# Kernel tuning notes

Measured on AMD Instinct MI355X. Metric: run time of the kernel, lower is better.

## Reference

```python
import jax, jax.numpy as jnp
import numpy as np

ROWS = 256
COLS = 256
EPS = 1e-8


def _radius_bins(rows, cols):
    # Same construction as SpectralLoss.__init__: integer radius per rfft bin,
    # ifftshifted along the row axis to match torch.rfft layout.
    shift_rows = rows // 2
    cols_onesided = cols // 2 + 1
    idx = np.indices((rows, cols_onesided)) - np.array([[[shift_rows]], [[0]]])
    r = np.sqrt(idx[0] ** 2 + idx[1] ** 2).astype(int)
    r = np.fft.ifftshift(r, axes=0)
    return r  # [rows, cols_onesided], values in [0, r_max]


def setup_inputs() -> dict:
    key = jax.random.key(0)
    k1, k2 = jax.random.split(key)
    r = _radius_bins(ROWS, COLS)
    vector_length = int(r.max()) + 1  # 182
    data = jax.random.normal(k1, (128, 3, ROWS, COLS), dtype=jnp.float32)
    mean = jax.random.uniform(k2, (vector_length,), dtype=jnp.float32)
    radius = jnp.asarray(r, dtype=jnp.int32)
    return {"data": data, "mean": mean, "radius": radius}


def reference(data, mean, radius):
    L = mean.shape[0]  # vector_length = r_max + 1
    # RGB -> luma (as in SpectralLoss.fft)
    gray = 0.299 * data[:, 0] + 0.587 * data[:, 1] + 0.114 * data[:, 2]  # [B,H,W]
    f = jnp.fft.rfft2(gray)  # [B, H, W//2+1]
    power = f.real ** 2 + f.imag ** 2  # sum of squared re/im parts
    fft_abs = 20.0 * jnp.log(power + EPS)  # [B, H, Wc]
    # Radial histogram: segment-mean keyed on integer radius (replaces the
    # original dense one-hot mask broadcast of shape [B, L, H, Wc]).
    seg = radius.reshape(-1)  # [N] with N = H*Wc
    B = fft_abs.shape[0]
    flat = fft_abs.reshape(B, -1).T  # [N, B]
    sums = jax.ops.segment_sum(flat, seg, num_segments=L)  # [L, B]
    counts = jax.ops.segment_sum(jnp.ones_like(flat[:, :1]), seg, num_segments=L)  # [L, 1]
    profile = (sums / counts).T  # [B, L]
    # Per-sample min-max normalization (same order of ops as torch code)
    profile = profile - jnp.min(profile, axis=1, keepdims=True)
    profile = profile / jnp.max(profile, axis=1, keepdims=True)
    # L1 loss with reduction='sum' against the target mean profile
    return jnp.sum(jnp.abs(profile - mean[None, :]))
```

## Files before the change

### kernel.cpp

```cpp
#include <hip/hip_runtime.h>
#include <cmath>

#define B_   128
#define H_   256
#define W_   256
#define WC_  129
#define L_   182
#define NG_  33
#define PI_F 3.14159265358979f

__device__ __forceinline__ void fft256_wave(float vr[4], float vi[4], int l) {
  float c0, s0;
  __sincosf(-2.f * PI_F * (float)l / 256.f, &s0, &c0);
  {
    float ur = vr[0] + vr[2], ui = vi[0] + vi[2];
    float dr = vr[0] - vr[2], di = vi[0] - vi[2];
    vr[0] = ur; vi[0] = ui;
    vr[2] = dr * c0 - di * s0; vi[2] = dr * s0 + di * c0;
    float c1 = s0, s1 = -c0;
    ur = vr[1] + vr[3]; ui = vi[1] + vi[3];
    dr = vr[1] - vr[3]; di = vi[1] - vi[3];
    vr[1] = ur; vi[1] = ui;
    vr[3] = dr * c1 - di * s1; vi[3] = dr * s1 + di * c1;
  }
  {
    float c2 = c0 * c0 - s0 * s0, s2 = 2.f * c0 * s0;
    float ur = vr[0] + vr[1], ui = vi[0] + vi[1];
    float dr = vr[0] - vr[1], di = vi[0] - vi[1];
    vr[0] = ur; vi[0] = ui;
    vr[1] = dr * c2 - di * s2; vi[1] = dr * s2 + di * c2;
    ur = vr[2] + vr[3]; ui = vi[2] + vi[3];
    dr = vr[2] - vr[3]; di = vi[2] - vi[3];
    vr[2] = ur; vi[2] = ui;
    vr[3] = dr * c2 - di * s2; vi[3] = dr * s2 + di * c2;
  }
  #pragma unroll
  for (int h = 32; h >= 1; h >>= 1) {
    int i = l & (h - 1);
    float c, s;
    __sincosf(-PI_F * (float)i / (float)h, &s, &c);
    bool up = (l & h) != 0;
    float cc = up ? c : 1.f;
    float ss = up ? s : 0.f;
    float sgn = up ? -1.f : 1.f;
    #pragma unroll
    for (int j = 0; j < 4; ++j) {
      float br = __shfl_xor(vr[j], h, 64);
      float bi = __shfl_xor(vi[j], h, 64);
      float tr = fmaf(sgn, vr[j], br);
      float ti = fmaf(sgn, vi[j], bi);
      vr[j] = tr * cc - ti * ss;
      vi[j] = tr * ss + ti * cc;
    }
  }
}

__device__ __forceinline__ void stage4(float (&vr)[4][4], float (&vi)[4][4],
                                       int l, int h, float CT, float ST) {
  int i = l & (h - 1);
  float s, c;
  __sincosf(-PI_F * (float)i / (float)h, &s, &c);
  float wr[4], wi[4];
  wr[0] = c;                    wi[0] = s;
  wr[1] = c * CT + s * ST;      wi[1] = s * CT - c * ST;
  wr[2] = wr[1] * CT + wi[1] * ST; wi[2] = wi[1] * CT - wr[1] * ST;
  wr[3] = wr[2] * CT + wi[2] * ST; wi[3] = wi[2] * CT - wr[2] * ST;
  bool up = (l & h) != 0;
  float sgn = up ? -1.f : 1.f;
  #pragma unroll
  for (int f = 0; f < 4; ++f) {
    #pragma unroll
    for (int j = 0; j < 4; ++j) {
      float br = __shfl_xor(vr[f][j], h, 64);
      float bi = __shfl_xor(vi[f][j], h, 64);
      float tr = fmaf(sgn, vr[f][j], br);
      float ti = fmaf(sgn, vi[f][j], bi);
      float cc = up ? wr[j] : 1.f;
      float ss = up ? wi[j] : 0.f;
      vr[f][j] = tr * cc - ti * ss;
      vi[f][j] = tr * ss + ti * cc;
    }
  }
}

__device__ __forceinline__ float4 luma4(float4 r, float4 g, float4 b) {
  float4 o;
  o.x = fmaf(0.299f, r.x, fmaf(0.587f, g.x, 0.114f * b.x));
  o.y = fmaf(0.299f, r.y, fmaf(0.587f, g.y, 0.114f * b.y));
  o.z = fmaf(0.299f, r.z, fmaf(0.587f, g.z, 0.114f * b.z));
  o.w = fmaf(0.299f, r.w, fmaf(0.587f, g.w, 0.114f * b.w));
  return o;
}

#define P1_STRIDE 259

__global__ __launch_bounds__(256) void pass1_kernel(
    const float* __restrict__ data, float4* __restrict__ inter4) {
  __shared__ float2 tile[16 * P1_STRIDE];
  int tid = threadIdx.x;
  int w = tid >> 6, l = tid & 63;
  int b = blockIdx.x >> 3;
  int rg = blockIdx.x & 7;
  int row0 = rg * 32;
  const float* img = data + ((size_t)b * 3) * (H_ * W_);
  float vr[4][4], vi[4][4];
  #pragma unroll
  for (int half = 0; half < 2; ++half) {
    float4 ra[2], ga[2], ba[2], rb[2], gb[2], bb[2];
    #pragma unroll
    for (int e = 0; e < 2; ++e) {
      int f = half * 2 + e;
      int rowA = row0 + 2 * (4 * w + f);
      const float* pA = img + (size_t)rowA * W_ + 4 * l;
      ra[e] = *(const float4*)(pA);
      ga[e] = *(const float4*)(pA + H_ * W_);
      ba[e] = *(const float4*)(pA + 2 * H_ * W_);
      rb[e] = *(const float4*)(pA + W_);
      gb[e] = *(const float4*)(pA + H_ * W_ + W_);
      bb[e] = *(const float4*)(pA + 2 * H_ * W_ + W_);
    }
    #pragma unroll
    for (int e = 0; e < 2; ++e) {
      int f = half * 2 + e;
      float4 A = luma4(ra[e], ga[e], ba[e]);
      float4 Bv = luma4(rb[e], gb[e], bb[e]);
      vr[f][0] = A.x; vr[f][1] = A.y; vr[f][2] = A.z; vr[f][3] = A.w;
      vi[f][0] = Bv.x; vi[f][1] = Bv.y; vi[f][2] = Bv.z; vi[f][3] = Bv.w;
    }
  }
  stage4(vr, vi, l, 32, 0.9996988187f, 0.0245412285f);
  stage4(vr, vi, l, 16, 0.9987954562f, 0.0490676743f);
  stage4(vr, vi, l,  8, 0.9951847267f, 0.0980171403f);
  stage4(vr, vi, l,  4, 0.9807852804f, 0.1950903220f);
  stage4(vr, vi, l,  2, 0.9238795325f, 0.3826834324f);
  stage4(vr, vi, l,  1, 0.7071067812f, 0.7071067812f);
  #pragma unroll
  for (int f = 0; f < 4; ++f) {
    float u0r = vr[f][0] + vr[f][2], u0i = vi[f][0] + vi[f][2];
    float v0r = vr[f][0] - vr[f][2], v0i = vi[f][0] - vi[f][2];
    float u1r = vr[f][1] + vr[f][3], u1i = vi[f][1] + vi[f][3];
    float d1r = vr[f][1] - vr[f][3], d1i = vi[f][1] - vi[f][3];
    float v1r = d1i, v1i = -d1r;
    vr[f][0] = u0r + u1r; vi[f][0] = u0i + u1i;
    vr[f][1] = u0r - u1r; vi[f][1] = u0i - u1i;
    vr[f][2] = v0r + v1r; vi[f][2] = v0i + v1i;
    vr[f][3] = v0r - v1r; vi[f][3] = v0i - v1i;
    int p = 4 * w + f;
    #pragma unroll
    for (int j = 0; j < 4; ++j)
      tile[p * P1_STRIDE + l + 64 * j] = make_float2(vr[f][j], vi[f][j]);
  }
  __syncthreads();
  for (int fi = tid; fi < WC_ * 16; fi += 256) {
    int k = fi >> 4;
    int p = fi & 15;
    int q  = (int)(__brev((unsigned)k) >> 24);
    int qn = (int)(__brev((unsigned)((256 - k) & 255)) >> 24);
    int qs  = (q >> 2)  + 64 * (q & 3);
    int qns = (qn >> 2) + 64 * (qn & 3);
    float2 Zk  = tile[p * P1_STRIDE + qs];
    float2 Znk = tile[p * P1_STRIDE + qns];
    float4 o;
    o.x = 0.5f * (Zk.x + Znk.x);
    o.y = 0.5f * (Zk.y - Znk.y);
    o.z = 0.5f * (Zk.y + Znk.y);
    o.w = 0.5f * (Znk.x - Zk.x);
    inter4[((((size_t)b * WC_ + k) * H_ + row0) >> 1) + p] = o;
  }
}

__global__ __launch_bounds__(256) void pass2_kernel(
    const float2* __restrict__ inter, const int* __restrict__ radius,
    float* __restrict__ partial, float* __restrict__ cntpart) {
  __shared__ float lbins[L_];
  __shared__ float lcnt[L_];
  int tid = threadIdx.x;
  int wv = tid >> 6, l = tid & 63;
  int b = blockIdx.x / NG_;
  int g = blockIdx.x - b * NG_;
  int k = g * 4 + wv;
  bool do_cnt = (b == 0);
  for (int i = tid; i < L_; i += 256) lbins[i] = 0.f;
  if (do_cnt)
    for (int i = tid; i < L_; i += 256) lcnt[i] = 0.f;
  __syncthreads();
  if (k < WC_) {
    const float2* p = inter + ((size_t)b * WC_ + k) * H_;
    float vr[4], vi[4];
    #pragma unroll
    for (int j = 0; j < 4; ++j) {
      float2 v = p[l + 64 * j];
      vr[j] = v.x; vi[j] = v.y;
    }
    fft256_wave(vr, vi, l);
    int rb = 4 * (int)(__brev((unsigned)l) >> 26);
    #pragma unroll
    for (int j = 0; j < 4; ++j) {
      int rf = rb + ((j == 1) ? 2 : (j == 2) ? 1 : j);
      int bin = radius[rf * WC_ + k];
      float pw = vr[j] * vr[j] + vi[j] * vi[j];
      float val = 20.f * __logf(pw + 1e-8f);
      atomicAdd(&lbins[bin], val);
      if (do_cnt) atomicAdd(&lcnt[bin], 1.f);
    }
  }
  __syncthreads();
  float* pp = partial + ((size_t)b * NG_ + g) * L_;
  for (int i = tid; i < L_; i += 256) pp[i] = lbins[i];
  if (do_cnt) {
    float* cp = cntpart + (size_t)g * L_;
    for (int i = tid; i < L_; i += 256) cp[i] = lcnt[i];
  }
}

__global__ __launch_bounds__(256) void loss_kernel(
    const float* __restrict__ partial, const float* __restrict__ cntpart,
    const float* __restrict__ mean, float* __restrict__ lpart) {
  int b = blockIdx.x;
  int t = threadIdx.x;
  __shared__ float prof[L_];
  __shared__ float red[256];
  float acc = 0.f, csum = 0.f;
  if (t < L_) {
    const float* pb = partial + (size_t)b * NG_ * L_;
    #pragma unroll 3
    for (int g = 0; g < NG_; ++g) {
      acc  += pb[g * L_ + t];
      csum += cntpart[g * L_ + t];
    }
    prof[t] = acc / csum;
  }
  __syncthreads();
  red[t] = (t < L_) ? prof[t] : INFINITY;
  __syncthreads();
  for (int s = 128; s > 0; s >>= 1) {
    if (t < s) red[t] = fminf(red[t], red[t + s]);
    __syncthreads();
  }
  float mn = red[0];
  __syncthreads();
  red[t] = (t < L_) ? (prof[t] - mn) : -INFINITY;
  __syncthreads();
  for (int s = 128; s > 0; s >>= 1) {
    if (t < s) red[t] = fmaxf(red[t], red[t + s]);
    __syncthreads();
  }
  float mx = red[0];
  __syncthreads();
  red[t] = (t < L_) ? fabsf((prof[t] - mn) / mx - mean[t]) : 0.f;
  __syncthreads();
  for (int s = 128; s > 0; s >>= 1) {
    if (t < s) red[t] += red[t + s];
    __syncthreads();
  }
  if (t == 0) lpart[b] = red[0];
}

__global__ __launch_bounds__(64) void final_kernel(
    const float* __restrict__ lpart, float* __restrict__ out) {
  int l = threadIdx.x;
  float v = lpart[l] + lpart[l + 64];
  #pragma unroll
  for (int h = 32; h >= 1; h >>= 1) v += __shfl_xor(v, h, 64);
  if (l == 0) out[0] = v;
}

extern "C" void kernel_launch(void* const* d_in, const int* in_sizes, int n_in,
                              void* d_out, int out_size, void* d_ws, size_t ws_size,
                              hipStream_t stream) {
  const float* data   = (const float*)d_in[0];
  const float* mean   = (const float*)d_in[1];
  const int*   radius = (const int*)d_in[2];
  float* out = (float*)d_out;

  float2* inter = (float2*)d_ws;
  size_t inter_bytes = (size_t)B_ * WC_ * H_ * sizeof(float2);
  float* partial = (float*)((char*)d_ws + inter_bytes);
  float* cntpart = partial + (size_t)B_ * NG_ * L_;
  float* lpart   = cntpart + (size_t)NG_ * L_;

  pass1_kernel<<<B_ * 8, 256, 0, stream>>>(data, (float4*)inter);
  pass2_kernel<<<B_ * NG_, 256, 0, stream>>>(inter, radius, partial, cntpart);
  loss_kernel<<<B_, 256, 0, stream>>>(partial, cntpart, mean, lpart);
  final_kernel<<<1, 64, 0, stream>>>(lpart, out);
}
```

Before: 196.8 us.

## Fuse row and column FFT passes into one kernel using shared-memory transpose

New measurement: 219.9 us. 1.12x slower.

```diff
diff --git a/kernel.cpp b/kernel.cpp
--- a/kernel.cpp
+++ b/kernel.cpp
@@ -6,54 +6,10 @@
 #define W_   256
 #define WC_  129
 #define L_   182
-#define NG_  33
 #define PI_F 3.14159265358979f
 
-__device__ __forceinline__ void fft256_wave(float vr[4], float vi[4], int l) {
-  float c0, s0;
-  __sincosf(-2.f * PI_F * (float)l / 256.f, &s0, &c0);
-  {
-    float ur = vr[0] + vr[2], ui = vi[0] + vi[2];
-    float dr = vr[0] - vr[2], di = vi[0] - vi[2];
-    vr[0] = ur; vi[0] = ui;
-    vr[2] = dr * c0 - di * s0; vi[2] = dr * s0 + di * c0;
-    float c1 = s0, s1 = -c0;
-    ur = vr[1] + vr[3]; ui = vi[1] + vi[3];
-    dr = vr[1] - vr[3]; di = vi[1] - vi[3];
-    vr[1] = ur; vi[1] = ui;
-    vr[3] = dr * c1 - di * s1; vi[3] = dr * s1 + di * c1;
-  }
-  {
-    float c2 = c0 * c0 - s0 * s0, s2 = 2.f * c0 * s0;
-    float ur = vr[0] + vr[1], ui = vi[0] + vi[1];
-    float dr = vr[0] - vr[1], di = vi[0] - vi[1];
-    vr[0] = ur; vi[0] = ui;
-    vr[1] = dr * c2 - di * s2; vi[1] = dr * s2 + di * c2;
-    ur = vr[2] + vr[3]; ui = vi[2] + vi[3];
-    dr = vr[2] - vr[3]; di = vi[2] - vi[3];
-    vr[2] = ur; vi[2] = ui;
-    vr[3] = dr * c2 - di * s2; vi[3] = dr * s2 + di * c2;
-  }
-  #pragma unroll
-  for (int h = 32; h >= 1; h >>= 1) {
-    int i = l & (h - 1);
-    float c, s;
-    __sincosf(-PI_F * (float)i / (float)h, &s, &c);
-    bool up = (l & h) != 0;
-    float cc = up ? c : 1.f;
-    float ss = up ? s : 0.f;
-    float sgn = up ? -1.f : 1.f;
-    #pragma unroll
-    for (int j = 0; j < 4; ++j) {
-      float br = __shfl_xor(vr[j], h, 64);
-      float bi = __shfl_xor(vi[j], h, 64);
-      float tr = fmaf(sgn, vr[j], br);
-      float ti = fmaf(sgn, vi[j], bi);
-      vr[j] = tr * cc - ti * ss;
-      vi[j] = tr * ss + ti * cc;
-    }
-  }
-}
+#define COLS_ELEMS (128 * 65)
+#define SMEM_BYTES (COLS_ELEMS * 16 + 2 * L_ * 4)
 
 __device__ __forceinline__ void stage4(float (&vr)[4][4], float (&vi)[4][4],
                                        int l, int h, float CT, float ST) {
@@ -61,8 +17,8 @@
   float s, c;
   __sincosf(-PI_F * (float)i / (float)h, &s, &c);
   float wr[4], wi[4];
-  wr[0] = c;                    wi[0] = s;
-  wr[1] = c * CT + s * ST;      wi[1] = s * CT - c * ST;
+  wr[0] = c;                       wi[0] = s;
+  wr[1] = c * CT + s * ST;         wi[1] = s * CT - c * ST;
   wr[2] = wr[1] * CT + wi[1] * ST; wi[2] = wi[1] * CT - wr[1] * ST;
   wr[3] = wr[2] * CT + wi[2] * ST; wi[3] = wi[2] * CT - wr[2] * ST;
   bool up = (l & h) != 0;
@@ -83,51 +39,8 @@
   }
 }
 
-__device__ __forceinline__ float4 luma4(float4 r, float4 g, float4 b) {
-  float4 o;
-  o.x = fmaf(0.299f, r.x, fmaf(0.587f, g.x, 0.114f * b.x));
-  o.y = fmaf(0.299f, r.y, fmaf(0.587f, g.y, 0.114f * b.y));
-  o.z = fmaf(0.299f, r.z, fmaf(0.587f, g.z, 0.114f * b.z));
-  o.w = fmaf(0.299f, r.w, fmaf(0.587f, g.w, 0.114f * b.w));
-  return o;
-}
-
-#define P1_STRIDE 259
-
-__global__ __launch_bounds__(256) void pass1_kernel(
-    const float* __restrict__ data, float4* __restrict__ inter4) {
-  __shared__ float2 tile[16 * P1_STRIDE];
-  int tid = threadIdx.x;
-  int w = tid >> 6, l = tid & 63;
-  int b = blockIdx.x >> 3;
-  int rg = blockIdx.x & 7;
-  int row0 = rg * 32;
-  const float* img = data + ((size_t)b * 3) * (H_ * W_);
-  float vr[4][4], vi[4][4];
-  #pragma unroll
-  for (int half = 0; half < 2; ++half) {
-    float4 ra[2], ga[2], ba[2], rb[2], gb[2], bb[2];
-    #pragma unroll
-    for (int e = 0; e < 2; ++e) {
-      int f = half * 2 + e;
-      int rowA = row0 + 2 * (4 * w + f);
-      const float* pA = img + (size_t)rowA * W_ + 4 * l;
-      ra[e] = *(const float4*)(pA);
-      ga[e] = *(const float4*)(pA + H_ * W_);
-      ba[e] = *(const float4*)(pA + 2 * H_ * W_);
-      rb[e] = *(const float4*)(pA + W_);
-      gb[e] = *(const float4*)(pA + H_ * W_ + W_);
-      bb[e] = *(const float4*)(pA + 2 * H_ * W_ + W_);
-    }
-    #pragma unroll
-    for (int e = 0; e < 2; ++e) {
-      int f = half * 2 + e;
-      float4 A = luma4(ra[e], ga[e], ba[e]);
-      float4 Bv = luma4(rb[e], gb[e], bb[e]);
-      vr[f][0] = A.x; vr[f][1] = A.y; vr[f][2] = A.z; vr[f][3] = A.w;
-      vi[f][0] = Bv.x; vi[f][1] = Bv.y; vi[f][2] = Bv.z; vi[f][3] = Bv.w;
-    }
-  }
+__device__ __forceinline__ void fft256x4(float (&vr)[4][4], float (&vi)[4][4],
+                                         int l) {
   stage4(vr, vi, l, 32, 0.9996988187f, 0.0245412285f);
   stage4(vr, vi, l, 16, 0.9987954562f, 0.0490676743f);
   stage4(vr, vi, l,  8, 0.9951847267f, 0.0980171403f);
@@ -145,71 +58,135 @@
     vr[f][1] = u0r - u1r; vi[f][1] = u0i - u1i;
     vr[f][2] = v0r + v1r; vi[f][2] = v0i + v1i;
     vr[f][3] = v0r - v1r; vi[f][3] = v0i - v1i;
-    int p = 4 * w + f;
-    #pragma unroll
-    for (int j = 0; j < 4; ++j)
-      tile[p * P1_STRIDE + l + 64 * j] = make_float2(vr[f][j], vi[f][j]);
-  }
-  __syncthreads();
-  for (int fi = tid; fi < WC_ * 16; fi += 256) {
-    int k = fi >> 4;
-    int p = fi & 15;
-    int q  = (int)(__brev((unsigned)k) >> 24);
-    int qn = (int)(__brev((unsigned)((256 - k) & 255)) >> 24);
-    int qs  = (q >> 2)  + 64 * (q & 3);
-    int qns = (qn >> 2) + 64 * (qn & 3);
-    float2 Zk  = tile[p * P1_STRIDE + qs];
-    float2 Znk = tile[p * P1_STRIDE + qns];
-    float4 o;
-    o.x = 0.5f * (Zk.x + Znk.x);
-    o.y = 0.5f * (Zk.y - Znk.y);
-    o.z = 0.5f * (Zk.y + Znk.y);
-    o.w = 0.5f * (Znk.x - Zk.x);
-    inter4[((((size_t)b * WC_ + k) * H_ + row0) >> 1) + p] = o;
-  }
-}
-
-__global__ __launch_bounds__(256) void pass2_kernel(
-    const float2* __restrict__ inter, const int* __restrict__ radius,
+  }
+}
+
+__device__ __forceinline__ float4 luma4(float4 r, float4 g, float4 b) {
+  float4 o;
+  o.x = fmaf(0.299f, r.x, fmaf(0.587f, g.x, 0.114f * b.x));
+  o.y = fmaf(0.299f, r.y, fmaf(0.587f, g.y, 0.114f * b.y));
+  o.z = fmaf(0.299f, r.z, fmaf(0.587f, g.z, 0.114f * b.z));
+  o.w = fmaf(0.299f, r.w, fmaf(0.587f, g.w, 0.114f * b.w));
+  return o;
+}
+
+__global__ __launch_bounds__(1024) void fused_kernel(
+    const float* __restrict__ data, const int* __restrict__ radius,
     float* __restrict__ partial, float* __restrict__ cntpart) {
-  __shared__ float lbins[L_];
-  __shared__ float lcnt[L_];
+  extern __shared__ char smem[];
+  float4* cols4 = (float4*)smem;
+  float* lbins = (float*)(smem + COLS_ELEMS * 16);
+  float* lcnt  = lbins + L_;
+
   int tid = threadIdx.x;
-  int wv = tid >> 6, l = tid & 63;
-  int b = blockIdx.x / NG_;
-  int g = blockIdx.x - b * NG_;
-  int k = g * 4 + wv;
-  bool do_cnt = (b == 0);
-  for (int i = tid; i < L_; i += 256) lbins[i] = 0.f;
-  if (do_cnt)
-    for (int i = tid; i < L_; i += 256) lcnt[i] = 0.f;
-  __syncthreads();
-  if (k < WC_) {
-    const float2* p = inter + ((size_t)b * WC_ + k) * H_;
-    float vr[4], vi[4];
-    #pragma unroll
-    for (int j = 0; j < 4; ++j) {
-      float2 v = p[l + 64 * j];
-      vr[j] = v.x; vi[j] = v.y;
-    }
-    fft256_wave(vr, vi, l);
-    int rb = 4 * (int)(__brev((unsigned)l) >> 26);
-    #pragma unroll
-    for (int j = 0; j < 4; ++j) {
-      int rf = rb + ((j == 1) ? 2 : (j == 2) ? 1 : j);
-      int bin = radius[rf * WC_ + k];
-      float pw = vr[j] * vr[j] + vi[j] * vi[j];
-      float val = 20.f * __logf(pw + 1e-8f);
-      atomicAdd(&lbins[bin], val);
-      if (do_cnt) atomicAdd(&lcnt[bin], 1.f);
-    }
-  }
-  __syncthreads();
-  float* pp = partial + ((size_t)b * NG_ + g) * L_;
-  for (int i = tid; i < L_; i += 256) pp[i] = lbins[i];
+  int w = tid >> 6, l = tid & 63;
+  int bid = blockIdx.x;
+  int b = bid >> 1;
+  int half = bid & 1;
+  int k0h = half ? 65 : 0;
+  int klcount = half ? 64 : 65;
+  bool do_cnt = (bid < 2);
+
+  for (int i = tid; i < L_; i += 1024) { lbins[i] = 0.f; lcnt[i] = 0.f; }
+
+  const float* img = data + ((size_t)b * 3) * (H_ * W_);
+  const int m = (int)(__brev((unsigned)l) >> 26);
+  const int m2 = (64 - m) & 63;
+  const int l2 = (int)(__brev((unsigned)m2) >> 26);
+  const int amap[4] = {0, 2, 1, 3};
+
+  #pragma unroll
+  for (int bt = 0; bt < 2; ++bt) {
+    float vr[4][4], vi[4][4];
+    #pragma unroll
+    for (int hb = 0; hb < 2; ++hb) {
+      float4 ra[2], ga[2], ba[2], rb[2], gb[2], bb[2];
+      #pragma unroll
+      for (int e = 0; e < 2; ++e) {
+        int f = hb * 2 + e;
+        int p = w * 8 + bt * 4 + f;
+        const float* pA = img + (size_t)(2 * p) * W_ + 4 * l;
+        ra[e] = *(const float4*)(pA);
+        ga[e] = *(const float4*)(pA + H_ * W_);
+        ba[e] = *(const float4*)(pA + 2 * H_ * W_);
+        rb[e] = *(const float4*)(pA + W_);
+        gb[e] = *(const float4*)(pA + H_ * W_ + W_);
+        bb[e] = *(const float4*)(pA + 2 * H_ * W_ + W_);
+      }
+      #pragma unroll
+      for (int e = 0; e < 2; ++e) {
+        int f = hb * 2 + e;
+        float4 A = luma4(ra[e], ga[e], ba[e]);
+        float4 Bv = luma4(rb[e], gb[e], bb[e]);
+        vr[f][0] = A.x; vr[f][1] = A.y; vr[f][2] = A.z; vr[f][3] = A.w;
+        vi[f][0] = Bv.x; vi[f][1] = Bv.y; vi[f][2] = Bv.z; vi[f][3] = Bv.w;
+      }
+    }
+    fft256x4(vr, vi, l);
+    #pragma unroll
+    for (int f = 0; f < 4; ++f) {
+      int p = w * 8 + bt * 4 + f;
+      #pragma unroll
+      for (int j = 0; j < 3; ++j) {
+        int k = (amap[j] << 6) | m;
+        float pr = __shfl(vr[f][3 - j], l2, 64);
+        float pi = __shfl(vi[f][3 - j], l2, 64);
+        if (l == 0) {
+          int js = (j < 2) ? j : (5 - j);
+          pr = vr[f][js]; pi = vi[f][js];
+        }
+        int kl = k - k0h;
+        if (kl >= 0 && kl < klcount) {
+          float4 o;
+          o.x = 0.5f * (vr[f][j] + pr);
+          o.y = 0.5f * (vi[f][j] - pi);
+          o.z = 0.5f * (vi[f][j] + pi);
+          o.w = 0.5f * (pr - vr[f][j]);
+          cols4[p * 65 + kl] = o;
+        }
+      }
+    }
+  }
+  __syncthreads();
+
+  int tmax = (klcount + 3) >> 2;
+  for (int t = w; t < tmax; t += 16) {
+    float vr[4][4], vi[4][4];
+    #pragma unroll
+    for (int ff = 0; ff < 4; ++ff) {
+      int kl = 4 * t + ff;
+      int klr = (kl < klcount) ? kl : 0;
+      float4 c0 = cols4[(2 * l) * 65 + klr];
+      float4 c1 = cols4[(2 * l + 1) * 65 + klr];
+      vr[ff][0] = c0.x; vi[ff][0] = c0.y;
+      vr[ff][1] = c0.z; vi[ff][1] = c0.w;
+      vr[ff][2] = c1.x; vi[ff][2] = c1.y;
+      vr[ff][3] = c1.z; vi[ff][3] = c1.w;
+    }
+    fft256x4(vr, vi, l);
+    #pragma unroll
+    for (int ff = 0; ff < 4; ++ff) {
+      int kl = 4 * t + ff;
+      if (kl < klcount) {
+        int kabs = k0h + kl;
+        #pragma unroll
+        for (int j = 0; j < 4; ++j) {
+          int frow = (amap[j] << 6) | m;
+          int bin = radius[frow * WC_ + kabs];
+          float pw = vr[ff][j] * vr[ff][j] + vi[ff][j] * vi[ff][j];
+          float val = 20.f * __logf(pw + 1e-8f);
+          atomicAdd(&lbins[bin], val);
+          if (do_cnt) atomicAdd(&lcnt[bin], 1.f);
+        }
+      }
+    }
+  }
+  __syncthreads();
+  float* pp = partial + (size_t)bid * L_;
+  for (int i = tid; i < L_; i += 1024) pp[i] = lbins[i];
   if (do_cnt) {
-    float* cp = cntpart + (size_t)g * L_;
-    for (int i = tid; i < L_; i += 256) cp[i] = lcnt[i];
+    float* cp = cntpart + (size_t)half * L_;
+    for (int i = tid; i < L_; i += 1024) cp[i] = lcnt[i];
   }
 }
 
@@ -220,14 +197,10 @@
   int t = threadIdx.x;
   __shared__ float prof[L_];
   __shared__ float red[256];
-  float acc = 0.f, csum = 0.f;
   if (t < L_) {
-    const float* pb = partial + (size_t)b * NG_ * L_;
-    #pragma unroll 3
-    for (int g = 0; g < NG_; ++g) {
-      acc  += pb[g * L_ + t];
-      csum += cntpart[g * L_ + t];
-    }
+    float acc  = partial[(size_t)(b * 2) * L_ + t] +
+                 partial[(size_t)(b * 2 + 1) * L_ + t];
+    float csum = cntpart[t] + cntpart[L_ + t];
     prof[t] = acc / csum;
   }
   __syncthreads();
@@ -273,14 +246,15 @@
   const int*   radius = (const int*)d_in[2];
   float* out = (float*)d_out;
 
-  float2* inter = (float2*)d_ws;
-  size_t inter_bytes = (size_t)B_ * WC_ * H_ * sizeof(float2);
-  float* partial = (float*)((char*)d_ws + inter_bytes);
-  float* cntpart = partial + (size_t)B_ * NG_ * L_;
-  float* lpart   = cntpart + (size_t)NG_ * L_;
-
-  pass1_kernel<<<B_ * 8, 256, 0, stream>>>(data, (float4*)inter);
-  pass2_kernel<<<B_ * NG_, 256, 0, stream>>>(inter, radius, partial, cntpart);
+  float* partial = (float*)d_ws;
+  float* cntpart = partial + (size_t)256 * L_;
+  float* lpart   = cntpart + 2 * L_;
+
+  (void)hipFuncSetAttribute((const void*)fused_kernel,
+                            hipFuncAttributeMaxDynamicSharedMemorySize,
+                            SMEM_BYTES);
+
+  fused_kernel<<<B_ * 2, 1024, SMEM_BYTES, stream>>>(data, radius, partial, cntpart);
   loss_kernel<<<B_, 256, 0, stream>>>(partial, cntpart, mean, lpart);
   final_kernel<<<1, 64, 0, stream>>>(lpart, out);
 }
```

## Store FFT intermediate in fp16, batch column FFTs, fuse loss into pass2

Applied to the files above, without the earlier changes.

Result: slower. 299.9 us (+52.4%).

```diff
diff --git a/kernel.cpp b/kernel.cpp
--- a/kernel.cpp
+++ b/kernel.cpp
@@ -6,54 +6,11 @@
 #define W_   256
 #define WC_  129
 #define L_   182
-#define NG_  33
+#define NG_  9
 #define PI_F 3.14159265358979f
 
-__device__ __forceinline__ void fft256_wave(float vr[4], float vi[4], int l) {
-  float c0, s0;
-  __sincosf(-2.f * PI_F * (float)l / 256.f, &s0, &c0);
-  {
-    float ur = vr[0] + vr[2], ui = vi[0] + vi[2];
-    float dr = vr[0] - vr[2], di = vi[0] - vi[2];
-    vr[0] = ur; vi[0] = ui;
-    vr[2] = dr * c0 - di * s0; vi[2] = dr * s0 + di * c0;
-    float c1 = s0, s1 = -c0;
-    ur = vr[1] + vr[3]; ui = vi[1] + vi[3];
-    dr = vr[1] - vr[3]; di = vi[1] - vi[3];
-    vr[1] = ur; vi[1] = ui;
-    vr[3] = dr * c1 - di * s1; vi[3] = dr * s1 + di * c1;
-  }
-  {
-    float c2 = c0 * c0 - s0 * s0, s2 = 2.f * c0 * s0;
-    float ur = vr[0] + vr[1], ui = vi[0] + vi[1];
-    float dr = vr[0] - vr[1], di = vi[0] - vi[1];
-    vr[0] = ur; vi[0] = ui;
-    vr[1] = dr * c2 - di * s2; vi[1] = dr * s2 + di * c2;
-    ur = vr[2] + vr[3]; ui = vi[2] + vi[3];
-    dr = vr[2] - vr[3]; di = vi[2] - vi[3];
-    vr[2] = ur; vi[2] = ui;
-    vr[3] = dr * c2 - di * s2; vi[3] = dr * s2 + di * c2;
-  }
-  #pragma unroll
-  for (int h = 32; h >= 1; h >>= 1) {
-    int i = l & (h - 1);
-    float c, s;
-    __sincosf(-PI_F * (float)i / (float)h, &s, &c);
-    bool up = (l & h) != 0;
-    float cc = up ? c : 1.f;
-    float ss = up ? s : 0.f;
-    float sgn = up ? -1.f : 1.f;
-    #pragma unroll
-    for (int j = 0; j < 4; ++j) {
-      float br = __shfl_xor(vr[j], h, 64);
-      float bi = __shfl_xor(vi[j], h, 64);
-      float tr = fmaf(sgn, vr[j], br);
-      float ti = fmaf(sgn, vi[j], bi);
-      vr[j] = tr * cc - ti * ss;
-      vi[j] = tr * ss + ti * cc;
-    }
-  }
-}
+using half4 = __attribute__((ext_vector_type(4))) _Float16;
+using half8 = __attribute__((ext_vector_type(8))) _Float16;
 
 __device__ __forceinline__ void stage4(float (&vr)[4][4], float (&vi)[4][4],
                                        int l, int h, float CT, float ST) {
@@ -61,8 +18,8 @@
   float s, c;
   __sincosf(-PI_F * (float)i / (float)h, &s, &c);
   float wr[4], wi[4];
-  wr[0] = c;                    wi[0] = s;
-  wr[1] = c * CT + s * ST;      wi[1] = s * CT - c * ST;
+  wr[0] = c;                       wi[0] = s;
+  wr[1] = c * CT + s * ST;         wi[1] = s * CT - c * ST;
   wr[2] = wr[1] * CT + wi[1] * ST; wi[2] = wi[1] * CT - wr[1] * ST;
   wr[3] = wr[2] * CT + wi[2] * ST; wi[3] = wi[2] * CT - wr[2] * ST;
   bool up = (l & h) != 0;
@@ -83,6 +40,28 @@
   }
 }
 
+__device__ __forceinline__ void fft256x4(float (&vr)[4][4], float (&vi)[4][4],
+                                         int l) {
+  stage4(vr, vi, l, 32, 0.9996988187f, 0.0245412285f);
+  stage4(vr, vi, l, 16, 0.9987954562f, 0.0490676743f);
+  stage4(vr, vi, l,  8, 0.9951847267f, 0.0980171403f);
+  stage4(vr, vi, l,  4, 0.9807852804f, 0.1950903220f);
+  stage4(vr, vi, l,  2, 0.9238795325f, 0.3826834324f);
+  stage4(vr, vi, l,  1, 0.7071067812f, 0.7071067812f);
+  #pragma unroll
+  for (int f = 0; f < 4; ++f) {
+    float u0r = vr[f][0] + vr[f][2], u0i = vi[f][0] + vi[f][2];
+    float v0r = vr[f][0] - vr[f][2], v0i = vi[f][0] - vi[f][2];
+    float u1r = vr[f][1] + vr[f][3], u1i = vi[f][1] + vi[f][3];
+    float d1r = vr[f][1] - vr[f][3], d1i = vi[f][1] - vi[f][3];
+    float v1r = d1i, v1i = -d1r;
+    vr[f][0] = u0r + u1r; vi[f][0] = u0i + u1i;
+    vr[f][1] = u0r - u1r; vi[f][1] = u0i - u1i;
+    vr[f][2] = v0r + v1r; vi[f][2] = v0i + v1i;
+    vr[f][3] = v0r - v1r; vi[f][3] = v0i - v1i;
+  }
+}
+
 __device__ __forceinline__ float4 luma4(float4 r, float4 g, float4 b) {
   float4 o;
   o.x = fmaf(0.299f, r.x, fmaf(0.587f, g.x, 0.114f * b.x));
@@ -95,9 +74,14 @@
 #define P1_STRIDE 259
 
 __global__ __launch_bounds__(256) void pass1_kernel(
-    const float* __restrict__ data, float4* __restrict__ inter4) {
+    const float* __restrict__ data, half4* __restrict__ interh,
+    const int* __restrict__ radius, float* __restrict__ cnt,
+    int* __restrict__ counters) {
   __shared__ float2 tile[16 * P1_STRIDE];
+  __shared__ float lcnt[L_];
   int tid = threadIdx.x;
+  bool blk0 = (blockIdx.x == 0);
+  if (blk0 && tid < L_) lcnt[tid] = 0.f;
   int w = tid >> 6, l = tid & 63;
   int b = blockIdx.x >> 3;
   int rg = blockIdx.x & 7;
@@ -128,23 +112,9 @@
       vi[f][0] = Bv.x; vi[f][1] = Bv.y; vi[f][2] = Bv.z; vi[f][3] = Bv.w;
     }
   }
-  stage4(vr, vi, l, 32, 0.9996988187f, 0.0245412285f);
-  stage4(vr, vi, l, 16, 0.9987954562f, 0.0490676743f);
-  stage4(vr, vi, l,  8, 0.9951847267f, 0.0980171403f);
-  stage4(vr, vi, l,  4, 0.9807852804f, 0.1950903220f);
-  stage4(vr, vi, l,  2, 0.9238795325f, 0.3826834324f);
-  stage4(vr, vi, l,  1, 0.7071067812f, 0.7071067812f);
+  fft256x4(vr, vi, l);
   #pragma unroll
   for (int f = 0; f < 4; ++f) {
-    float u0r = vr[f][0] + vr[f][2], u0i = vi[f][0] + vi[f][2];
-    float v0r = vr[f][0] - vr[f][2], v0i = vi[f][0] - vi[f][2];
-    float u1r = vr[f][1] + vr[f][3], u1i = vi[f][1] + vi[f][3];
-    float d1r = vr[f][1] - vr[f][3], d1i = vi[f][1] - vi[f][3];
-    float v1r = d1i, v1i = -d1r;
-    vr[f][0] = u0r + u1r; vi[f][0] = u0i + u1i;
-    vr[f][1] = u0r - u1r; vi[f][1] = u0i - u1i;
-    vr[f][2] = v0r + v1r; vi[f][2] = v0i + v1i;
-    vr[f][3] = v0r - v1r; vi[f][3] = v0i - v1i;
     int p = 4 * w + f;
     #pragma unroll
     for (int j = 0; j < 4; ++j)
@@ -160,109 +130,126 @@
     int qns = (qn >> 2) + 64 * (qn & 3);
     float2 Zk  = tile[p * P1_STRIDE + qs];
     float2 Znk = tile[p * P1_STRIDE + qns];
-    float4 o;
-    o.x = 0.5f * (Zk.x + Znk.x);
-    o.y = 0.5f * (Zk.y - Znk.y);
-    o.z = 0.5f * (Zk.y + Znk.y);
-    o.w = 0.5f * (Znk.x - Zk.x);
-    inter4[((((size_t)b * WC_ + k) * H_ + row0) >> 1) + p] = o;
+    half4 o;
+    o[0] = (_Float16)(0.5f * (Zk.x + Znk.x));
+    o[1] = (_Float16)(0.5f * (Zk.y - Znk.y));
+    o[2] = (_Float16)(0.5f * (Zk.y + Znk.y));
+    o[3] = (_Float16)(0.5f * (Znk.x - Zk.x));
+    interh[((size_t)b * WC_ + k) * 128 + rg * 16 + p] = o;
+  }
+  if (blk0) {
+    __syncthreads();
+    int base = tid * 129;
+    int end  = base + 129;
+    if (end > H_ * WC_) end = H_ * WC_;
+    for (int i = base; i < end; ++i) atomicAdd(&lcnt[radius[i]], 1.f);
+    __syncthreads();
+    if (tid < L_) cnt[tid] = lcnt[tid];
+    if (tid < B_ + 1) counters[tid] = 0;
   }
 }
 
 __global__ __launch_bounds__(256) void pass2_kernel(
-    const float2* __restrict__ inter, const int* __restrict__ radius,
-    float* __restrict__ partial, float* __restrict__ cntpart) {
+    const half8* __restrict__ interh8, const int* __restrict__ radius,
+    const float* __restrict__ cnt, const float* __restrict__ mean,
+    float* __restrict__ partial, float* __restrict__ lpart,
+    int* __restrict__ counters, float* __restrict__ out) {
   __shared__ float lbins[L_];
-  __shared__ float lcnt[L_];
+  __shared__ float prof[L_];
+  __shared__ float red[256];
+  __shared__ int flag;
   int tid = threadIdx.x;
   int wv = tid >> 6, l = tid & 63;
   int b = blockIdx.x / NG_;
   int g = blockIdx.x - b * NG_;
-  int k = g * 4 + wv;
-  bool do_cnt = (b == 0);
   for (int i = tid; i < L_; i += 256) lbins[i] = 0.f;
-  if (do_cnt)
-    for (int i = tid; i < L_; i += 256) lcnt[i] = 0.f;
-  __syncthreads();
-  if (k < WC_) {
-    const float2* p = inter + ((size_t)b * WC_ + k) * H_;
-    float vr[4], vi[4];
-    #pragma unroll
-    for (int j = 0; j < 4; ++j) {
-      float2 v = p[l + 64 * j];
-      vr[j] = v.x; vi[j] = v.y;
-    }
-    fft256_wave(vr, vi, l);
-    int rb = 4 * (int)(__brev((unsigned)l) >> 26);
-    #pragma unroll
-    for (int j = 0; j < 4; ++j) {
-      int rf = rb + ((j == 1) ? 2 : (j == 2) ? 1 : j);
-      int bin = radius[rf * WC_ + k];
-      float pw = vr[j] * vr[j] + vi[j] * vi[j];
-      float val = 20.f * __logf(pw + 1e-8f);
-      atomicAdd(&lbins[bin], val);
-      if (do_cnt) atomicAdd(&lcnt[bin], 1.f);
+  __syncthreads();
+
+  const int amap[4] = {0, 2, 1, 3};
+  const int m = (int)(__brev((unsigned)l) >> 26);
+  float vr[4][4], vi[4][4];
+  int kc[4];
+  #pragma unroll
+  for (int ff = 0; ff < 4; ++ff) {
+    int k = g * 16 + wv * 4 + ff;
+    kc[ff] = k;
+    int kr = (k < WC_) ? k : 0;
+    half8 hx = interh8[((size_t)b * WC_ + kr) * 64 + l];
+    vr[ff][0] = (float)hx[0]; vi[ff][0] = (float)hx[1];
+    vr[ff][1] = (float)hx[2]; vi[ff][1] = (float)hx[3];
+    vr[ff][2] = (float)hx[4]; vi[ff][2] = (float)hx[5];
+    vr[ff][3] = (float)hx[6]; vi[ff][3] = (float)hx[7];
+  }
+  fft256x4(vr, vi, l);
+  #pragma unroll
+  for (int ff = 0; ff < 4; ++ff) {
+    if (kc[ff] < WC_) {
+      #pragma unroll
+      for (int j = 0; j < 4; ++j) {
+        int frow = (amap[j] << 6) | m;
+        int bin = radius[frow * WC_ + kc[ff]];
+        float pw = vr[ff][j] * vr[ff][j] + vi[ff][j] * vi[ff][j];
+        atomicAdd(&lbins[bin], 20.f * __logf(pw + 1e-8f));
+      }
     }
   }
   __syncthreads();
   float* pp = partial + ((size_t)b * NG_ + g) * L_;
   for (int i = tid; i < L_; i += 256) pp[i] = lbins[i];
-  if (do_cnt) {
-    float* cp = cntpart + (size_t)g * L_;
-    for (int i = tid; i < L_; i += 256) cp[i] = lcnt[i];
-  }
-}
-
-__global__ __launch_bounds__(256) void loss_kernel(
-    const float* __restrict__ partial, const float* __restrict__ cntpart,
-    const float* __restrict__ mean, float* __restrict__ lpart) {
-  int b = blockIdx.x;
-  int t = threadIdx.x;
-  __shared__ float prof[L_];
-  __shared__ float red[256];
-  float acc = 0.f, csum = 0.f;
-  if (t < L_) {
+
+  if (tid == 0) {
+    __threadfence();
+    flag = (atomicAdd(&counters[b], 1) == NG_ - 1) ? 1 : 0;
+  }
+  __syncthreads();
+  if (!flag) return;
+  __threadfence();
+  if (tid < L_) {
     const float* pb = partial + (size_t)b * NG_ * L_;
-    #pragma unroll 3
-    for (int g = 0; g < NG_; ++g) {
-      acc  += pb[g * L_ + t];
-      csum += cntpart[g * L_ + t];
-    }
-    prof[t] = acc / csum;
-  }
-  __syncthreads();
-  red[t] = (t < L_) ? prof[t] : INFINITY;
-  __syncthreads();
-  for (int s = 128; s > 0; s >>= 1) {
-    if (t < s) red[t] = fminf(red[t], red[t + s]);
+    float acc = 0.f;
+    #pragma unroll
+    for (int gg = 0; gg < NG_; ++gg) acc += pb[gg * L_ + tid];
+    prof[tid] = acc / cnt[tid];
+  }
+  __syncthreads();
+  red[tid] = (tid < L_) ? prof[tid] : INFINITY;
+  __syncthreads();
+  for (int s = 128; s > 0; s >>= 1) {
+    if (tid < s) red[tid] = fminf(red[tid], red[tid + s]);
     __syncthreads();
   }
   float mn = red[0];
   __syncthreads();
-  red[t] = (t < L_) ? (prof[t] - mn) : -INFINITY;
-  __syncthreads();
-  for (int s = 128; s > 0; s >>= 1) {
-    if (t < s) red[t] = fmaxf(red[t], red[t + s]);
+  red[tid] = (tid < L_) ? (prof[tid] - mn) : -INFINITY;
+  __syncthreads();
+  for (int s = 128; s > 0; s >>= 1) {
+    if (tid < s) red[tid] = fmaxf(red[tid], red[tid + s]);
     __syncthreads();
   }
   float mx = red[0];
   __syncthreads();
-  red[t] = (t < L_) ? fabsf((prof[t] - mn) / mx - mean[t]) : 0.f;
-  __syncthreads();
-  for (int s = 128; s > 0; s >>= 1) {
-    if (t < s) red[t] += red[t + s];
-    __syncthreads();
-  }
-  if (t == 0) lpart[b] = red[0];
-}
-
-__global__ __launch_bounds__(64) void final_kernel(
-    const float* __restrict__ lpart, float* __restrict__ out) {
-  int l = threadIdx.x;
-  float v = lpart[l] + lpart[l + 64];
-  #pragma unroll
-  for (int h = 32; h >= 1; h >>= 1) v += __shfl_xor(v, h, 64);
-  if (l == 0) out[0] = v;
+  red[tid] = (tid < L_) ? fabsf((prof[tid] - mn) / mx - mean[tid]) : 0.f;
+  __syncthreads();
+  for (int s = 128; s > 0; s >>= 1) {
+    if (tid < s) red[tid] += red[tid + s];
+    __syncthreads();
+  }
+  if (tid == 0) lpart[b] = red[0];
+
+  if (tid == 0) {
+    __threadfence();
+    flag = (atomicAdd(&counters[B_], 1) == B_ - 1) ? 1 : 0;
+  }
+  __syncthreads();
+  if (!flag) return;
+  __threadfence();
+  red[tid] = (tid < B_) ? lpart[tid] : 0.f;
+  __syncthreads();
+  for (int s = 128; s > 0; s >>= 1) {
+    if (tid < s) red[tid] += red[tid + s];
+    __syncthreads();
+  }
+  if (tid == 0) out[0] = red[0];
 }
 
 extern "C" void kernel_launch(void* const* d_in, const int* in_sizes, int n_in,
@@ -273,14 +260,14 @@
   const int*   radius = (const int*)d_in[2];
   float* out = (float*)d_out;
 
-  float2* inter = (float2*)d_ws;
-  size_t inter_bytes = (size_t)B_ * WC_ * H_ * sizeof(float2);
-  float* partial = (float*)((char*)d_ws + inter_bytes);
-  float* cntpart = partial + (size_t)B_ * NG_ * L_;
-  float* lpart   = cntpart + (size_t)NG_ * L_;
-
-  pass1_kernel<<<B_ * 8, 256, 0, stream>>>(data, (float4*)inter);
-  pass2_kernel<<<B_ * NG_, 256, 0, stream>>>(inter, radius, partial, cntpart);
-  loss_kernel<<<B_, 256, 0, stream>>>(partial, cntpart, mean, lpart);
-  final_kernel<<<1, 64, 0, stream>>>(lpart, out);
-}
+  half4* interh = (half4*)d_ws;
+  size_t inter_bytes = (size_t)B_ * WC_ * 128 * sizeof(half4);
+  float* partial  = (float*)((char*)d_ws + inter_bytes);
+  float* cnt      = partial + (size_t)B_ * NG_ * L_;
+  float* lpart    = cnt + L_;
+  int*   counters = (int*)(lpart + B_);
+
+  pass1_kernel<<<B_ * 8, 256, 0, stream>>>(data, interh, radius, cnt, counters);
+  pass2_kernel<<<B_ * NG_, 256, 0, stream>>>((const half8*)interh, radius, cnt,
+                                             mean, partial, lpart, counters, out);
+}
```
